# Performance work log

Hardware: AMD Instinct MI355X
Metric: run time of the kernel (lower is better)

The kernel has to match this reference:

```python
import jax, jax.numpy as jnp
import numpy as np

DIM = 2048
N_HEADS = 16
HEAD_DIM = DIM // N_HEADS
HIDDEN = ((int(DIM * 4 * 2 / 3) + 63) // 64) * 64  # 5504, per SwiGLUFFN __init__
B, T = 2, 2048
LN_EPS = 1e-5


def layer_norm(x, g, b):
    m = jnp.mean(x, axis=-1, keepdims=True)
    v = jnp.mean(jnp.square(x - m), axis=-1, keepdims=True)
    return (x - m) * jax.lax.rsqrt(v + LN_EPS) * g + b


def apply_rope(x, cos, sin):
    # x: [B, T, H, D]; cos/sin: [T, D//2]
    d = x.shape[-1]
    x1, x2 = x[..., : d // 2], x[..., d // 2:]
    c = cos[None, :, None, :]
    s = sin[None, :, None, :]
    return jnp.concatenate([x1 * c - x2 * s, x1 * s + x2 * c], axis=-1)


def setup_inputs() -> dict:
    key = jax.random.key(0)
    ks = jax.random.split(key, 8)
    x = jax.random.normal(ks[0], (B, T, DIM), dtype=jnp.float32)
    # RoPE tables (standard inv-freq construction)
    inv_freq = 1.0 / (10000.0 ** (np.arange(0, HEAD_DIM, 2, dtype=np.float32) / HEAD_DIM))
    t = np.arange(T, dtype=np.float32)
    freqs = np.outer(t, inv_freq)  # [T, D//2]
    cos = jnp.asarray(np.cos(freqs))
    sin = jnp.asarray(np.sin(freqs))
    # causal additive mask [T, T]
    mask = jnp.where(jnp.tril(jnp.ones((T, T), dtype=bool)), 0.0, -1e9).astype(jnp.float32)
    sc = 0.02
    params = dict(
        ln1_g=jnp.ones((DIM,), jnp.float32), ln1_b=jnp.zeros((DIM,), jnp.float32),
        ln2_g=jnp.ones((DIM,), jnp.float32), ln2_b=jnp.zeros((DIM,), jnp.float32),
        w_qkv=jax.random.normal(ks[1], (DIM, 3 * DIM), jnp.float32) * sc,
        w_out=jax.random.normal(ks[2], (DIM, DIM), jnp.float32) * sc,
        w_gate=jax.random.normal(ks[3], (DIM, 2 * HIDDEN), jnp.float32) * sc,
        w_down=jax.random.normal(ks[4], (HIDDEN, DIM), jnp.float32) * sc,
    )
    return dict(x=x, cos=cos, sin=sin, mask=mask, **params)


def reference(x, cos, sin, mask, ln1_g, ln1_b, ln2_g, ln2_b, w_qkv, w_out, w_gate, w_down):
    Bx, Tx, C = x.shape
    scale = HEAD_DIM ** -0.5
    # ---- attention branch ----
    h = layer_norm(x, ln1_g, ln1_b)
    qkv = (h @ w_qkv).reshape(Bx, Tx, 3, N_HEADS, HEAD_DIM)
    q, k, v = qkv[:, :, 0], qkv[:, :, 1], qkv[:, :, 2]  # [B,T,H,D]
    q = apply_rope(q, cos, sin)
    k = apply_rope(k, cos, sin)
    attn = jnp.einsum('bqhd,bkhd->bhqk', q, k) * scale
    attn = attn + mask[None, None, :, :]
    attn = jax.nn.softmax(attn, axis=-1)
    o = jnp.einsum('bhqk,bkhd->bqhd', attn, v).reshape(Bx, Tx, C)
    x = x + o @ w_out
    # ---- SwiGLU FFN branch ----
    h = layer_norm(x, ln2_g, ln2_b)
    gv = h @ w_gate
    g, vv = gv[..., :HIDDEN], gv[..., HIDDEN:]
    x = x + (jax.nn.silu(g) * vv) @ w_down
    return x
```

## Files before the change

### kernel.cpp

```cpp
#include <hip/hip_runtime.h>

#define DIM 2048
#define NH 16
#define HD 128
#define HIDDEN 5504
#define BB 2
#define TT 2048
#define M_ROWS (BB*TT)
#define QKV_N (3*DIM)
#define ATT_SCALE 0.08838834764831845f

typedef float f32x4 __attribute__((ext_vector_type(4)));
typedef __bf16 bf16x8 __attribute__((ext_vector_type(8)));

__device__ __forceinline__ float bf2f(unsigned short u){
  unsigned x = ((unsigned)u) << 16; float f; __builtin_memcpy(&f, &x, 4); return f;
}
__device__ __forceinline__ unsigned short f2bf(float f){
  unsigned x; __builtin_memcpy(&x, &f, 4);
  x = (x + 0x7fffu + ((x >> 16) & 1u)) >> 16;
  return (unsigned short)x;
}

__global__ __launch_bounds__(256) void k_transpose(const float* __restrict__ src,
                                                   unsigned short* __restrict__ dst,
                                                   int K, int N){
  __shared__ float tile[64][65];
  int nb = blockIdx.x * 64, kb = blockIdx.y * 64;
  int tid = threadIdx.x, c = tid & 63, r0 = tid >> 6;
  #pragma unroll
  for (int i = 0; i < 16; i++){
    int r = i * 4 + r0;
    tile[r][c] = src[(size_t)(kb + r) * N + nb + c];
  }
  __syncthreads();
  #pragma unroll
  for (int i = 0; i < 16; i++){
    int r = i * 4 + r0;
    dst[(size_t)(nb + r) * K + kb + c] = f2bf(tile[c][r]);
  }
}

__global__ __launch_bounds__(256) void k_vtrans(const unsigned short* __restrict__ qkv,
                                                unsigned short* __restrict__ Vt_g){
  int bh = blockIdx.z; int b = bh >> 4, h = bh & 15;
  int tb = blockIdx.x * 64, db = blockIdx.y * 64;
  const unsigned short* Vp = qkv + (size_t)b * TT * QKV_N + 2 * DIM + h * HD;
  __shared__ unsigned short tile[64][66];
  int tid = threadIdx.x, c = tid & 63, r0 = tid >> 6;
  #pragma unroll
  for (int i = 0; i < 16; i++){
    int r = i * 4 + r0;
    tile[r][c] = Vp[(size_t)(tb + r) * QKV_N + db + c];
  }
  __syncthreads();
  #pragma unroll
  for (int i = 0; i < 16; i++){
    int r = i * 4 + r0;
    Vt_g[((size_t)bh * HD + db + r) * TT + tb + c] = tile[c][r];
  }
}

__global__ __launch_bounds__(256) void k_ln(const float* __restrict__ x,
                                            const float* __restrict__ g,
                                            const float* __restrict__ b,
                                            unsigned short* __restrict__ out){
  int row = blockIdx.x, tid = threadIdx.x;
  const float* xr = x + (size_t)row * DIM;
  int c0 = tid * 4, c1 = 1024 + tid * 4;
  float4 a = *(const float4*)(xr + c0);
  float4 c = *(const float4*)(xr + c1);
  float s  = a.x + a.y + a.z + a.w + c.x + c.y + c.z + c.w;
  float sq = a.x*a.x + a.y*a.y + a.z*a.z + a.w*a.w + c.x*c.x + c.y*c.y + c.z*c.z + c.w*c.w;
  #pragma unroll
  for (int off = 1; off < 64; off <<= 1){
    s  += __shfl_xor(s,  off);
    sq += __shfl_xor(sq, off);
  }
  __shared__ float red[8];
  int wave = tid >> 6;
  if ((tid & 63) == 0){ red[wave] = s; red[4 + wave] = sq; }
  __syncthreads();
  s  = red[0] + red[1] + red[2] + red[3];
  sq = red[4] + red[5] + red[6] + red[7];
  float mean = s * (1.f / DIM);
  float var  = sq * (1.f / DIM) - mean * mean;
  float rs   = rsqrtf(var + 1e-5f);
  float4 g0 = *(const float4*)(g + c0), g1 = *(const float4*)(g + c1);
  float4 b0 = *(const float4*)(b + c0), b1 = *(const float4*)(b + c1);
  ushort4 o0, o1;
  o0.x = f2bf((a.x - mean) * rs * g0.x + b0.x);
  o0.y = f2bf((a.y - mean) * rs * g0.y + b0.y);
  o0.z = f2bf((a.z - mean) * rs * g0.z + b0.z);
  o0.w = f2bf((a.w - mean) * rs * g0.w + b0.w);
  o1.x = f2bf((c.x - mean) * rs * g1.x + b1.x);
  o1.y = f2bf((c.y - mean) * rs * g1.y + b1.y);
  o1.z = f2bf((c.z - mean) * rs * g1.z + b1.z);
  o1.w = f2bf((c.w - mean) * rs * g1.w + b1.w);
  *(ushort4*)(out + (size_t)row * DIM + c0) = o0;
  *(ushort4*)(out + (size_t)row * DIM + c1) = o1;
}

template<int EPI>
__global__ __launch_bounds__(256) void k_gemm(const unsigned short* __restrict__ A,
                                              const unsigned short* __restrict__ Bt,
                                              unsigned short* __restrict__ Cb,
                                              const float* __restrict__ res,
                                              float* __restrict__ Cf,
                                              int M, int N, int K){
  __shared__ __align__(16) unsigned short As[128][72];
  __shared__ __align__(16) unsigned short Bs[128][72];
  int tid = threadIdx.x;
  int wave = tid >> 6, lane = tid & 63, lg = lane >> 4, lr = lane & 15;
  int wm = wave >> 1, wn = wave & 1;
  int m0 = blockIdx.y * 128, n0 = blockIdx.x * 128;
  f32x4 acc[4][4];
  #pragma unroll
  for (int mi = 0; mi < 4; mi++)
    #pragma unroll
    for (int nj = 0; nj < 4; nj++)
      acc[mi][nj] = (f32x4)0.f;
  int srow = tid >> 3, scol = (tid & 7) * 8;
  for (int k0 = 0; k0 < K; k0 += 64){
    __syncthreads();
    #pragma unroll
    for (int i = 0; i < 4; i++){
      int r = srow + i * 32;
      *(int4*)(&As[r][scol]) = *(const int4*)(A  + (size_t)(m0 + r) * K + k0 + scol);
      *(int4*)(&Bs[r][scol]) = *(const int4*)(Bt + (size_t)(n0 + r) * K + k0 + scol);
    }
    __syncthreads();
    #pragma unroll
    for (int kk = 0; kk < 2; kk++){
      bf16x8 af[4], bfr[4];
      #pragma unroll
      for (int mi = 0; mi < 4; mi++)
        af[mi] = *(const bf16x8*)(&As[wm * 64 + mi * 16 + lr][kk * 32 + lg * 8]);
      #pragma unroll
      for (int nj = 0; nj < 4; nj++)
        bfr[nj] = *(const bf16x8*)(&Bs[wn * 64 + nj * 16 + lr][kk * 32 + lg * 8]);
      #pragma unroll
      for (int mi = 0; mi < 4; mi++)
        #pragma unroll
        for (int nj = 0; nj < 4; nj++)
          acc[mi][nj] = __builtin_amdgcn_mfma_f32_16x16x32_bf16(af[mi], bfr[nj], acc[mi][nj], 0, 0, 0);
    }
  }
  #pragma unroll
  for (int mi = 0; mi < 4; mi++){
    #pragma unroll
    for (int r = 0; r < 4; r++){
      int m = m0 + wm * 64 + mi * 16 + lg * 4 + r;
      #pragma unroll
      for (int nj = 0; nj < 4; nj++){
        int n = n0 + wn * 64 + nj * 16 + lr;
        if (EPI == 0)
          Cb[(size_t)m * N + n] = f2bf(acc[mi][nj][r]);
        else
          Cf[(size_t)m * N + n] = res[(size_t)m * N + n] + acc[mi][nj][r];
      }
    }
  }
}

__global__ __launch_bounds__(256) void k_rope(unsigned short* __restrict__ qkv,
                                              const float* __restrict__ cosp,
                                              const float* __restrict__ sinp){
  int gid = blockIdx.x * 256 + threadIdx.x;
  int m = gid >> 10;
  int rem = gid & 1023;
  int h = rem >> 6, d = rem & 63;
  int t = m & (TT - 1);
  size_t base = (size_t)m * QKV_N + h * HD;
  float c = cosp[t * 64 + d], s = sinp[t * 64 + d];
  float q1 = bf2f(qkv[base + d]), q2 = bf2f(qkv[base + 64 + d]);
  qkv[base + d]      = f2bf((q1 * c - q2 * s) * ATT_SCALE);
  qkv[base + 64 + d] = f2bf((q1 * s + q2 * c) * ATT_SCALE);
  size_t kb = base + DIM;
  float k1 = bf2f(qkv[kb + d]), k2 = bf2f(qkv[kb + 64 + d]);
  qkv[kb + d]      = f2bf(k1 * c - k2 * s);
  qkv[kb + 64 + d] = f2bf(k1 * s + k2 * c);
}

__global__ __launch_bounds__(256) void k_attn(const unsigned short* __restrict__ qkv,
                                              const unsigned short* __restrict__ Vt_g,
                                              unsigned short* __restrict__ O){
  int qb = blockIdx.x;
  int bh = blockIdx.y;
  int b = bh >> 4, h = bh & 15;
  const unsigned short* Qp = qkv + (size_t)b * TT * QKV_N + h * HD;
  const unsigned short* Kp = Qp + DIM;
  __shared__ __align__(16) unsigned short Kt[64][136];
  __shared__ __align__(16) unsigned short Vt[128][72];
  __shared__ __align__(16) unsigned short Ps[4][32][72];
  int tid = threadIdx.x, wave = tid >> 6, lane = tid & 63, lg = lane >> 4, lr = lane & 15;
  int q0 = qb * 128 + wave * 32;
  bf16x8 qf[2][4];
  #pragma unroll
  for (int mi = 0; mi < 2; mi++)
    #pragma unroll
    for (int dc = 0; dc < 4; dc++)
      qf[mi][dc] = *(const bf16x8*)(Qp + (size_t)(q0 + mi * 16 + lr) * QKV_N + dc * 32 + lg * 8);
  f32x4 of[2][8];
  #pragma unroll
  for (int mi = 0; mi < 2; mi++)
    #pragma unroll
    for (int dj = 0; dj < 8; dj++)
      of[mi][dj] = (f32x4)0.f;
  float mrun[2] = {-1e30f, -1e30f}, lrun[2] = {0.f, 0.f};
  int ktmax = 2 * qb + 1;
  int sr = tid >> 4, sc8 = (tid & 15) * 8;
  int vr = tid >> 3, vc8 = (tid & 7) * 8;
  for (int kt = 0; kt <= ktmax; kt++){
    int kbase = kt * 64;
    __syncthreads();
    #pragma unroll
    for (int i = 0; i < 4; i++){
      int rr = sr + i * 16;
      *(int4*)(&Kt[rr][sc8]) = *(const int4*)(Kp + (size_t)(kbase + rr) * QKV_N + sc8);
      int dd = vr + i * 32;
      *(int4*)(&Vt[dd][vc8]) = *(const int4*)(Vt_g + ((size_t)bh * HD + dd) * TT + kbase + vc8);
    }
    __syncthreads();
    f32x4 st[4][2];
    #pragma unroll
    for (int kj = 0; kj < 4; kj++)
      #pragma unroll
      for (int mi = 0; mi < 2; mi++)
        st[kj][mi] = (f32x4)0.f;
    #pragma unroll
    for (int kj = 0; kj < 4; kj++){
      #pragma unroll
      for (int dc = 0; dc < 4; dc++){
        bf16x8 kf = *(const bf16x8*)(&Kt[kj * 16 + lr][dc * 32 + lg * 8]);
        st[kj][0] = __builtin_amdgcn_mfma_f32_16x16x32_bf16(kf, qf[0][dc], st[kj][0], 0, 0, 0);
        st[kj][1] = __builtin_amdgcn_mfma_f32_16x16x32_bf16(kf, qf[1][dc], st[kj][1], 0, 0, 0);
      }
    }
    #pragma unroll
    for (int kj = 0; kj < 4; kj++){
      int kg = kbase + kj * 16 + lg * 4;
      #pragma unroll
      for (int mi = 0; mi < 2; mi++){
        int qg = q0 + mi * 16 + lr;
        #pragma unroll
        for (int r = 0; r < 4; r++)
          if (kg + r > qg) st[kj][mi][r] = -1e30f;
      }
    }
    #pragma unroll
    for (int mi = 0; mi < 2; mi++){
      float mx = -1e30f;
      #pragma unroll
      for (int kj = 0; kj < 4; kj++)
        #pragma unroll
        for (int r = 0; r < 4; r++)
          mx = fmaxf(mx, st[kj][mi][r]);
      mx = fmaxf(mx, __shfl_xor(mx, 16));
      mx = fmaxf(mx, __shfl_xor(mx, 32));
      float mnew = fmaxf(mrun[mi], mx);
      float fsc = __expf(mrun[mi] - mnew);
      float rs = 0.f;
      #pragma unroll
      for (int kj = 0; kj < 4; kj++)
        #pragma unroll
        for (int r = 0; r < 4; r++){
          float p = __expf(st[kj][mi][r] - mnew);
          st[kj][mi][r] = p;
          rs += p;
        }
      rs += __shfl_xor(rs, 16);
      rs += __shfl_xor(rs, 32);
      lrun[mi] = lrun[mi] * fsc + rs;
      mrun[mi] = mnew;
      float fr[4];
      #pragma unroll
      for (int r = 0; r < 4; r++) fr[r] = __shfl(fsc, lg * 4 + r);
      #pragma unroll
      for (int dj = 0; dj < 8; dj++)
        #pragma unroll
        for (int r = 0; r < 4; r++)
          of[mi][dj][r] *= fr[r];
      #pragma unroll
      for (int kj = 0; kj < 4; kj++){
        ushort4 pk;
        pk.x = f2bf(st[kj][mi][0]);
        pk.y = f2bf(st[kj][mi][1]);
        pk.z = f2bf(st[kj][mi][2]);
        pk.w = f2bf(st[kj][mi][3]);
        *(ushort4*)(&Ps[wave][mi * 16 + lr][kj * 16 + lg * 4]) = pk;
      }
    }
    #pragma unroll
    for (int kc = 0; kc < 2; kc++){
      bf16x8 pf0 = *(const bf16x8*)(&Ps[wave][lr][kc * 32 + lg * 8]);
      bf16x8 pf1 = *(const bf16x8*)(&Ps[wave][16 + lr][kc * 32 + lg * 8]);
      #pragma unroll
      for (int dj = 0; dj < 8; dj++){
        bf16x8 vf = *(const bf16x8*)(&Vt[dj * 16 + lr][kc * 32 + lg * 8]);
        of[0][dj] = __builtin_amdgcn_mfma_f32_16x16x32_bf16(pf0, vf, of[0][dj], 0, 0, 0);
        of[1][dj] = __builtin_amdgcn_mfma_f32_16x16x32_bf16(pf1, vf, of[1][dj], 0, 0, 0);
      }
    }
  }
  #pragma unroll
  for (int mi = 0; mi < 2; mi++){
    float inv[4];
    #pragma unroll
    for (int r = 0; r < 4; r++) inv[r] = 1.f / __shfl(lrun[mi], lg * 4 + r);
    #pragma unroll
    for (int r = 0; r < 4; r++){
      int t = q0 + mi * 16 + lg * 4 + r;
      size_t rowb = ((size_t)b * TT + t) * DIM + h * HD;
      #pragma unroll
      for (int dj = 0; dj < 8; dj++)
        O[rowb + dj * 16 + lr] = f2bf(of[mi][dj][r] * inv[r]);
    }
  }
}

__global__ __launch_bounds__(256) void k_silu(const unsigned short* __restrict__ gv,
                                              unsigned short* __restrict__ act){
  int gid = blockIdx.x * 256 + threadIdx.x;
  unsigned m = (unsigned)gid / 688u;
  int j8 = (gid - (int)m * 688) * 8;
  const unsigned short* gp = gv + (size_t)m * (2 * HIDDEN) + j8;
  union { int4 v; unsigned short s[8]; } G, V, Ov;
  G.v = *(const int4*)(gp);
  V.v = *(const int4*)(gp + HIDDEN);
  #pragma unroll
  for (int j = 0; j < 8; j++){
    float g = bf2f(G.s[j]);
    float v = bf2f(V.s[j]);
    float sg = g / (1.f + __expf(-g));
    Ov.s[j] = f2bf(sg * v);
  }
  *(int4*)(act + (size_t)m * HIDDEN + j8) = Ov.v;
}

extern "C" void kernel_launch(void* const* d_in, const int* in_sizes, int n_in,
                              void* d_out, int out_size, void* d_ws, size_t ws_size,
                              hipStream_t stream){
  const float* x     = (const float*)d_in[0];
  const float* cosp  = (const float*)d_in[1];
  const float* sinp  = (const float*)d_in[2];
  const float* ln1g  = (const float*)d_in[4];
  const float* ln1b  = (const float*)d_in[5];
  const float* ln2g  = (const float*)d_in[6];
  const float* ln2b  = (const float*)d_in[7];
  const float* wqkv  = (const float*)d_in[8];
  const float* wout  = (const float*)d_in[9];
  const float* wgate = (const float*)d_in[10];
  const float* wdown = (const float*)d_in[11];
  float* outp = (float*)d_out;

  char* ws = (char*)d_ws;
  size_t off = 0;
  auto alloc = [&](size_t bytes) -> void* {
    void* p = ws + off;
    off += (bytes + 255) & ~(size_t)255;
    return p;
  };
  unsigned short* wqkvT  = (unsigned short*)alloc((size_t)QKV_N * DIM * 2);
  unsigned short* woutT  = (unsigned short*)alloc((size_t)DIM * DIM * 2);
  unsigned short* wgateT = (unsigned short*)alloc((size_t)2 * HIDDEN * DIM * 2);
  unsigned short* wdownT = (unsigned short*)alloc((size_t)DIM * HIDDEN * 2);
  float*          x1     = (float*)alloc((size_t)M_ROWS * DIM * 4);
  unsigned short* h1     = (unsigned short*)alloc((size_t)M_ROWS * DIM * 2);
  unsigned short* h2     = (unsigned short*)alloc((size_t)M_ROWS * DIM * 2);
  unsigned short* act    = (unsigned short*)alloc((size_t)M_ROWS * HIDDEN * 2);
  unsigned short* Vt_g   = (unsigned short*)alloc((size_t)BB * NH * HD * TT * 2);
  unsigned short* big    = (unsigned short*)alloc((size_t)M_ROWS * 2 * HIDDEN * 2);
  unsigned short* qkvb = big;
  unsigned short* gvb  = big;
  unsigned short* Obuf = h1;
  (void)ws_size; (void)in_sizes; (void)n_in; (void)out_size;

  k_transpose<<<dim3(QKV_N / 64, DIM / 64), 256, 0, stream>>>(wqkv, wqkvT, DIM, QKV_N);
  k_transpose<<<dim3(DIM / 64, DIM / 64), 256, 0, stream>>>(wout, woutT, DIM, DIM);
  k_transpose<<<dim3(2 * HIDDEN / 64, DIM / 64), 256, 0, stream>>>(wgate, wgateT, DIM, 2 * HIDDEN);
  k_transpose<<<dim3(DIM / 64, HIDDEN / 64), 256, 0, stream>>>(wdown, wdownT, HIDDEN, DIM);
  k_ln<<<M_ROWS, 256, 0, stream>>>(x, ln1g, ln1b, h1);
  k_gemm<0><<<dim3(QKV_N / 128, M_ROWS / 128), 256, 0, stream>>>(h1, wqkvT, qkvb, nullptr, nullptr, M_ROWS, QKV_N, DIM);
  k_rope<<<(M_ROWS * NH * 64) / 256, 256, 0, stream>>>(qkvb, cosp, sinp);
  k_vtrans<<<dim3(TT / 64, HD / 64, BB * NH), 256, 0, stream>>>(qkvb, Vt_g);
  k_attn<<<dim3(TT / 128, BB * NH), 256, 0, stream>>>(qkvb, Vt_g, Obuf);
  k_gemm<1><<<dim3(DIM / 128, M_ROWS / 128), 256, 0, stream>>>(Obuf, woutT, nullptr, x, x1, M_ROWS, DIM, DIM);
  k_ln<<<M_ROWS, 256, 0, stream>>>(x1, ln2g, ln2b, h2);
  k_gemm<0><<<dim3(2 * HIDDEN / 128, M_ROWS / 128), 256, 0, stream>>>(h2, wgateT, gvb, nullptr, nullptr, M_ROWS, 2 * HIDDEN, DIM);
  k_silu<<<(M_ROWS * (HIDDEN / 8)) / 256, 256, 0, stream>>>(gvb, act);
  k_gemm<1><<<dim3(DIM / 128, M_ROWS / 128), 256, 0, stream>>>(act, wdownT, nullptr, x1, outp, M_ROWS, DIM, HIDDEN);
}
```

Measured before the change: 1.036 ms.

## Replace GEMM with 256x256 double-buffered direct-to-LDS MFMA kernel

All four projection GEMMs move from a 128x128, 4-wave, single-buffered kernel to a 256x256, 8-wave kernel. The new kernel loads global memory straight into LDS via global_load_lds into a double buffer, so loads for the next k-tile overlap MFMA work on the current one. It also adds an XOR swizzle against LDS bank conflicts, s_setprio around MFMA bursts, and an XCD-aware remapping of workgroup ids for L2 locality. The cost is a 128KB LDS footprint (one block per CU), many barriers, and coarser tiles that may leave CUs idle on the smaller N=2048 GEMMs.

New measurement: 975.6 us. 5.8% less time.

```diff
diff --git a/kernel.cpp b/kernel.cpp
--- a/kernel.cpp
+++ b/kernel.cpp
@@ -13,6 +13,9 @@
 typedef float f32x4 __attribute__((ext_vector_type(4)));
 typedef __bf16 bf16x8 __attribute__((ext_vector_type(8)));
 
+#define AS1 __attribute__((address_space(1)))
+#define AS3 __attribute__((address_space(3)))
+
 __device__ __forceinline__ float bf2f(unsigned short u){
   unsigned x = ((unsigned)u) << 16; float f; __builtin_memcpy(&f, &x, 4); return f;
 }
@@ -20,6 +23,10 @@
   unsigned x; __builtin_memcpy(&x, &f, 4);
   x = (x + 0x7fffu + ((x >> 16) & 1u)) >> 16;
   return (unsigned short)x;
+}
+__device__ __forceinline__ void gl_lds16(const unsigned short* g, unsigned short* l){
+  __builtin_amdgcn_global_load_lds((AS1 const void*)(uintptr_t)g,
+                                   (AS3 void*)(unsigned int)(uintptr_t)l, 16, 0, 0);
 }
 
 __global__ __launch_bounds__(256) void k_transpose(const float* __restrict__ src,
@@ -102,58 +109,150 @@
 }
 
 template<int EPI>
-__global__ __launch_bounds__(256) void k_gemm(const unsigned short* __restrict__ A,
-                                              const unsigned short* __restrict__ Bt,
-                                              unsigned short* __restrict__ Cb,
-                                              const float* __restrict__ res,
-                                              float* __restrict__ Cf,
-                                              int M, int N, int K){
-  __shared__ __align__(16) unsigned short As[128][72];
-  __shared__ __align__(16) unsigned short Bs[128][72];
-  int tid = threadIdx.x;
-  int wave = tid >> 6, lane = tid & 63, lg = lane >> 4, lr = lane & 15;
-  int wm = wave >> 1, wn = wave & 1;
-  int m0 = blockIdx.y * 128, n0 = blockIdx.x * 128;
-  f32x4 acc[4][4];
-  #pragma unroll
-  for (int mi = 0; mi < 4; mi++)
+__global__ __launch_bounds__(512, 2) void k_gemm8(const unsigned short* __restrict__ A,
+                                                  const unsigned short* __restrict__ Bt,
+                                                  unsigned short* __restrict__ Cb,
+                                                  const float* __restrict__ res,
+                                                  float* __restrict__ Cf,
+                                                  int M, int N, int K, int ntn){
+  __shared__ unsigned short lds[2][2][256 * 64];
+  const int tid  = threadIdx.x;
+  const int wave = tid >> 6, l = tid & 63;
+  const int lg = l >> 4, lr = l & 15;
+  const int wm = wave >> 2, wn = wave & 3;
+
+  const int nwg = gridDim.x;
+  const int q8 = nwg >> 3, r8 = nwg & 7;
+  const int xcd = blockIdx.x & 7, loc = blockIdx.x >> 3;
+  const int wgid = (xcd < r8 ? xcd * (q8 + 1) : r8 * (q8 + 1) + (xcd - r8) * q8) + loc;
+  const int tm = wgid / ntn, tn = wgid - tm * ntn;
+  const int m0 = tm * 256, n0 = tn * 256;
+
+  const int srow  = wave * 8 + (l >> 3);
+  const int sslot = (l & 7) ^ ((l >> 3) & 7);
+  const unsigned short* a_st = A  + (size_t)(m0 + srow) * K + sslot * 8;
+  const unsigned short* b_st = Bt + (size_t)(n0 + srow) * K + sslot * 8;
+  const int wch = wave * 64 * 8;
+
+  f32x4 acc[8][4];
+  #pragma unroll
+  for (int i = 0; i < 8; i++)
+    #pragma unroll
+    for (int j = 0; j < 4; j++) acc[i][j] = (f32x4)0.f;
+
+  const int ktiles = K >> 6;
+  char* base = (char*)&lds[0][0][0];
+
+  {
+    unsigned short* A0 = (unsigned short*)(base);
+    unsigned short* B0 = (unsigned short*)(base + 32768);
+    #pragma unroll
+    for (int h = 0; h < 2; h++)
+      #pragma unroll
+      for (int qq = 0; qq < 2; qq++){
+        gl_lds16(a_st + (size_t)(h * 128 + qq * 64) * K, A0 + (h * 1024 + qq * 512) * 8 + wch);
+        gl_lds16(b_st + (size_t)(h * 128 + qq * 64) * K, B0 + (h * 1024 + qq * 512) * 8 + wch);
+      }
+  }
+  asm volatile("s_waitcnt vmcnt(0)" ::: "memory");
+  __builtin_amdgcn_s_barrier();
+
+  const unsigned swz = (unsigned)((lr & 7) << 4);
+  const int arow = wm * 128 + lr;
+  const int brow = wn * 64 + lr;
+
+  for (int kt = 0; kt < ktiles; ++kt){
+    const int cur = kt & 1;
+    const char* Ab = base + cur * 65536;
+    const char* Bb = Ab + 32768;
+    unsigned short* Sa = (unsigned short*)(base + (cur ^ 1) * 65536);
+    unsigned short* Sb = (unsigned short*)((char*)Sa + 32768);
+    const size_t kpos = (size_t)((kt + 1 < ktiles) ? kt + 1 : kt) * 64;
+    const unsigned short* ag = a_st + kpos;
+    const unsigned short* bg = b_st + kpos;
+    bf16x8 a[4], b[4];
+
+    #pragma unroll
+    for (int mi = 0; mi < 4; mi++)
+      a[mi] = *(const bf16x8*)(Ab + (arow + mi * 16) * 128 + ((lg * 16) ^ swz));
     #pragma unroll
     for (int nj = 0; nj < 4; nj++)
-      acc[mi][nj] = (f32x4)0.f;
-  int srow = tid >> 3, scol = (tid & 7) * 8;
-  for (int k0 = 0; k0 < K; k0 += 64){
-    __syncthreads();
-    #pragma unroll
-    for (int i = 0; i < 4; i++){
-      int r = srow + i * 32;
-      *(int4*)(&As[r][scol]) = *(const int4*)(A  + (size_t)(m0 + r) * K + k0 + scol);
-      *(int4*)(&Bs[r][scol]) = *(const int4*)(Bt + (size_t)(n0 + r) * K + k0 + scol);
-    }
-    __syncthreads();
-    #pragma unroll
-    for (int kk = 0; kk < 2; kk++){
-      bf16x8 af[4], bfr[4];
-      #pragma unroll
-      for (int mi = 0; mi < 4; mi++)
-        af[mi] = *(const bf16x8*)(&As[wm * 64 + mi * 16 + lr][kk * 32 + lg * 8]);
+      b[nj] = *(const bf16x8*)(Bb + (brow + nj * 16) * 128 + ((lg * 16) ^ swz));
+    gl_lds16(ag,                      Sa + wch);
+    gl_lds16(ag + (size_t) 64 * K,    Sa + 512 * 8 + wch);
+    gl_lds16(ag + (size_t)128 * K,    Sa + 1024 * 8 + wch);
+    gl_lds16(ag + (size_t)192 * K,    Sa + 1536 * 8 + wch);
+    gl_lds16(bg,                      Sb + wch);
+    gl_lds16(bg + (size_t) 64 * K,    Sb + 512 * 8 + wch);
+    __builtin_amdgcn_s_barrier();
+    asm volatile("s_waitcnt lgkmcnt(0)" ::: "memory");
+    __builtin_amdgcn_s_setprio(1);
+    #pragma unroll
+    for (int mi = 0; mi < 4; mi++)
       #pragma unroll
       for (int nj = 0; nj < 4; nj++)
-        bfr[nj] = *(const bf16x8*)(&Bs[wn * 64 + nj * 16 + lr][kk * 32 + lg * 8]);
-      #pragma unroll
-      for (int mi = 0; mi < 4; mi++)
-        #pragma unroll
-        for (int nj = 0; nj < 4; nj++)
-          acc[mi][nj] = __builtin_amdgcn_mfma_f32_16x16x32_bf16(af[mi], bfr[nj], acc[mi][nj], 0, 0, 0);
-    }
-  }
-  #pragma unroll
-  for (int mi = 0; mi < 4; mi++){
+        acc[mi][nj] = __builtin_amdgcn_mfma_f32_16x16x32_bf16(a[mi], b[nj], acc[mi][nj], 0, 0, 0);
+    __builtin_amdgcn_s_setprio(0);
+    __builtin_amdgcn_s_barrier();
+
+    #pragma unroll
+    for (int mi = 0; mi < 4; mi++)
+      a[mi] = *(const bf16x8*)(Ab + (arow + 64 + mi * 16) * 128 + ((lg * 16) ^ swz));
+    gl_lds16(bg + (size_t)128 * K,    Sb + 1024 * 8 + wch);
+    gl_lds16(bg + (size_t)192 * K,    Sb + 1536 * 8 + wch);
+    __builtin_amdgcn_s_barrier();
+    asm volatile("s_waitcnt lgkmcnt(0)" ::: "memory");
+    __builtin_amdgcn_s_setprio(1);
+    #pragma unroll
+    for (int mi = 0; mi < 4; mi++)
+      #pragma unroll
+      for (int nj = 0; nj < 4; nj++)
+        acc[4 + mi][nj] = __builtin_amdgcn_mfma_f32_16x16x32_bf16(a[mi], b[nj], acc[4 + mi][nj], 0, 0, 0);
+    __builtin_amdgcn_s_setprio(0);
+    __builtin_amdgcn_s_barrier();
+
+    #pragma unroll
+    for (int mi = 0; mi < 4; mi++)
+      a[mi] = *(const bf16x8*)(Ab + (arow + mi * 16) * 128 + ((64 + lg * 16) ^ swz));
+    #pragma unroll
+    for (int nj = 0; nj < 4; nj++)
+      b[nj] = *(const bf16x8*)(Bb + (brow + nj * 16) * 128 + ((64 + lg * 16) ^ swz));
+    __builtin_amdgcn_s_barrier();
+    asm volatile("s_waitcnt lgkmcnt(0)" ::: "memory");
+    __builtin_amdgcn_s_setprio(1);
+    #pragma unroll
+    for (int mi = 0; mi < 4; mi++)
+      #pragma unroll
+      for (int nj = 0; nj < 4; nj++)
+        acc[mi][nj] = __builtin_amdgcn_mfma_f32_16x16x32_bf16(a[mi], b[nj], acc[mi][nj], 0, 0, 0);
+    __builtin_amdgcn_s_setprio(0);
+    __builtin_amdgcn_s_barrier();
+
+    #pragma unroll
+    for (int mi = 0; mi < 4; mi++)
+      a[mi] = *(const bf16x8*)(Ab + (arow + 64 + mi * 16) * 128 + ((64 + lg * 16) ^ swz));
+    __builtin_amdgcn_s_barrier();
+    asm volatile("s_waitcnt lgkmcnt(0)" ::: "memory");
+    __builtin_amdgcn_s_setprio(1);
+    #pragma unroll
+    for (int mi = 0; mi < 4; mi++)
+      #pragma unroll
+      for (int nj = 0; nj < 4; nj++)
+        acc[4 + mi][nj] = __builtin_amdgcn_mfma_f32_16x16x32_bf16(a[mi], b[nj], acc[4 + mi][nj], 0, 0, 0);
+    __builtin_amdgcn_s_setprio(0);
+    asm volatile("s_waitcnt vmcnt(0)" ::: "memory");
+    __builtin_amdgcn_s_barrier();
+  }
+
+  #pragma unroll
+  for (int mi = 0; mi < 8; mi++){
+    const int mrow = m0 + wm * 128 + mi * 16 + lg * 4;
     #pragma unroll
     for (int r = 0; r < 4; r++){
-      int m = m0 + wm * 64 + mi * 16 + lg * 4 + r;
+      const int m = mrow + r;
       #pragma unroll
       for (int nj = 0; nj < 4; nj++){
-        int n = n0 + wn * 64 + nj * 16 + lr;
+        const int n = n0 + wn * 64 + nj * 16 + lr;
         if (EPI == 0)
           Cb[(size_t)m * N + n] = f2bf(acc[mi][nj][r]);
         else
@@ -381,13 +480,13 @@
   k_transpose<<<dim3(2 * HIDDEN / 64, DIM / 64), 256, 0, stream>>>(wgate, wgateT, DIM, 2 * HIDDEN);
   k_transpose<<<dim3(DIM / 64, HIDDEN / 64), 256, 0, stream>>>(wdown, wdownT, HIDDEN, DIM);
   k_ln<<<M_ROWS, 256, 0, stream>>>(x, ln1g, ln1b, h1);
-  k_gemm<0><<<dim3(QKV_N / 128, M_ROWS / 128), 256, 0, stream>>>(h1, wqkvT, qkvb, nullptr, nullptr, M_ROWS, QKV_N, DIM);
+  k_gemm8<0><<<(M_ROWS / 256) * (QKV_N / 256), 512, 0, stream>>>(h1, wqkvT, qkvb, nullptr, nullptr, M_ROWS, QKV_N, DIM, QKV_N / 256);
   k_rope<<<(M_ROWS * NH * 64) / 256, 256, 0, stream>>>(qkvb, cosp, sinp);
   k_vtrans<<<dim3(TT / 64, HD / 64, BB * NH), 256, 0, stream>>>(qkvb, Vt_g);
   k_attn<<<dim3(TT / 128, BB * NH), 256, 0, stream>>>(qkvb, Vt_g, Obuf);
-  k_gemm<1><<<dim3(DIM / 128, M_ROWS / 128), 256, 0, stream>>>(Obuf, woutT, nullptr, x, x1, M_ROWS, DIM, DIM);
+  k_gemm8<1><<<(M_ROWS / 256) * (DIM / 256), 512, 0, stream>>>(Obuf, woutT, nullptr, x, x1, M_ROWS, DIM, DIM, DIM / 256);
   k_ln<<<M_ROWS, 256, 0, stream>>>(x1, ln2g, ln2b, h2);
-  k_gemm<0><<<dim3(2 * HIDDEN / 128, M_ROWS / 128), 256, 0, stream>>>(h2, wgateT, gvb, nullptr, nullptr, M_ROWS, 2 * HIDDEN, DIM);
+  k_gemm8<0><<<(M_ROWS / 256) * (2 * HIDDEN / 256), 512, 0, stream>>>(h2, wgateT, gvb, nullptr, nullptr, M_ROWS, 2 * HIDDEN, DIM, 2 * HIDDEN / 256);
   k_silu<<<(M_ROWS * (HIDDEN / 8)) / 256, 256, 0, stream>>>(gvb, act);
-  k_gemm<1><<<dim3(DIM / 128, M_ROWS / 128), 256, 0, stream>>>(act, wdownT, nullptr, x1, outp, M_ROWS, DIM, HIDDEN);
-}
+  k_gemm8<1><<<(M_ROWS / 256) * (DIM / 256), 512, 0, stream>>>(act, wdownT, nullptr, x1, outp, M_ROWS, DIM, HIDDEN, DIM / 256);
+}
```
